# Optimization experiments

Measured on AMD Instinct MI355X. Metric: run time of the kernel, lower is better.

The kernel has to match this reference:

```python
import jax, jax.numpy as jnp
import numpy as np
from jax import lax

B, CIN, H, W = 2, 512, 64, 64
CD = CIN // 2            # down_dim = 256
CQ = CD // 8             # q/k channels = 32
EPS = 1e-5               # BatchNorm eps


def _conv3(x, w, b):
    # 3x3 conv, stride 1, padding 1 (init padding=1), NCHW/OIHW
    y = lax.conv_general_dilated(x, w, (1, 1), [(1, 1), (1, 1)],
                                 dimension_numbers=('NCHW', 'OIHW', 'NCHW'))
    return y + b[None, :, None, None]


def _bn(x, g, b, m, v):
    scale = g / jnp.sqrt(v + EPS)
    return x * scale[None, :, None, None] + (b - m * scale)[None, :, None, None]


def _prelu(x, a):
    return jnp.where(x > 0, x, a * x)


def _p1(x, w, b):
    # 1x1 conv as channel matmul
    return jnp.einsum('bchw,oc->bohw', x, w) + b[None, :, None, None]


def setup_inputs() -> dict:
    key = jax.random.key(0)
    it = iter(jax.random.split(key, 64))
    def nrm(shape, s=0.05):
        return jax.random.normal(next(it), shape, jnp.float32) * s
    inp = {
        'input_rgb': jax.random.normal(next(it), (B, CIN, H, W), jnp.float32),
        'input_dsm': jax.random.normal(next(it), (B, CIN, H, W), jnp.float32),
    }
    for m in ('rgb', 'dsm'):
        inp['conv_w_' + m] = nrm((CD, CIN, 3, 3))
        inp['conv_b_' + m] = nrm((CD,))
        inp['bn_g_' + m] = 1.0 + nrm((CD,))
        inp['bn_b_' + m] = nrm((CD,))
        inp['bn_m_' + m] = nrm((CD,))
        inp['bn_v_' + m] = jax.random.uniform(next(it), (CD,), jnp.float32, 0.5, 1.5)
        inp['prelu_' + m] = jnp.float32(0.25)
        inp['q_w_' + m] = nrm((CQ, CD)); inp['q_b_' + m] = nrm((CQ,))
        inp['k_w_' + m] = nrm((CQ, CD)); inp['k_b_' + m] = nrm((CQ,))
        inp['v_w_' + m] = nrm((CD, CD)); inp['v_b_' + m] = nrm((CD,))
        inp['up_w_' + m] = nrm((CIN, CD)); inp['up_b_' + m] = nrm((CIN,))
        inp['gamma_' + m] = jnp.float32(0.1)  # learned residual gate (zero-init in torch)
    return inp


def reference(input_rgb, input_dsm,
              conv_w_rgb, conv_b_rgb, bn_g_rgb, bn_b_rgb, bn_m_rgb, bn_v_rgb, prelu_rgb,
              q_w_rgb, q_b_rgb, k_w_rgb, k_b_rgb, v_w_rgb, v_b_rgb, up_w_rgb, up_b_rgb, gamma_rgb,
              conv_w_dsm, conv_b_dsm, bn_g_dsm, bn_b_dsm, bn_m_dsm, bn_v_dsm, prelu_dsm,
              q_w_dsm, q_b_dsm, k_w_dsm, k_b_dsm, v_w_dsm, v_b_dsm, up_w_dsm, up_b_dsm, gamma_dsm):
    conv_rgb = _prelu(_bn(_conv3(input_rgb, conv_w_rgb, conv_b_rgb),
                          bn_g_rgb, bn_b_rgb, bn_m_rgb, bn_v_rgb), prelu_rgb)
    conv_dsm = _prelu(_bn(_conv3(input_dsm, conv_w_dsm, conv_b_dsm),
                          bn_g_dsm, bn_b_dsm, bn_m_dsm, bn_v_dsm), prelu_dsm)
    b, c, h, w = conv_rgb.shape
    n = h * w
    q_rgb = _p1(conv_rgb, q_w_rgb, q_b_rgb).reshape(b, CQ, n)
    k_rgb = _p1(conv_rgb, k_w_rgb, k_b_rgb).reshape(b, CQ, n)
    v_rgb = _p1(conv_rgb, v_w_rgb, v_b_rgb).reshape(b, c, n)
    q_dsm = _p1(conv_dsm, q_w_dsm, q_b_dsm).reshape(b, CQ, n)
    k_dsm = _p1(conv_dsm, k_w_dsm, k_b_dsm).reshape(b, CQ, n)
    v_dsm = _p1(conv_dsm, v_w_dsm, v_b_dsm).reshape(b, c, n)
    # cross-modal unscaled attention: dsm queries attend over rgb keys
    attn_rgb = jax.nn.softmax(jnp.einsum('bqn,bqm->bnm', q_dsm, k_rgb), axis=-1)  # [b,n,n]
    o_rgb = jnp.einsum('bcj,bij->bci', v_rgb, attn_rgb).reshape(b, c, h, w)
    o_rgb = gamma_rgb * o_rgb + conv_rgb
    attn_dsm = jax.nn.softmax(jnp.einsum('bqn,bqm->bnm', q_rgb, k_dsm), axis=-1)
    o_dsm = jnp.einsum('bcj,bij->bci', v_dsm, attn_dsm).reshape(b, c, h, w)
    o_dsm = gamma_dsm * o_dsm + conv_dsm
    out_rgb = _p1(o_rgb, up_w_rgb, up_b_rgb) + input_rgb
    out_dsm = _p1(o_dsm, up_w_dsm, up_b_dsm) + input_dsm
    return (out_rgb, out_dsm)
```

## Files before the change

kernel.cpp:

```cpp
#include <hip/hip_runtime.h>
#include <hip/hip_bf16.h>
#include <stdint.h>


constexpr int CINCH = 512;
constexpr int NPIX  = 4096;

typedef __bf16 bf16x8 __attribute__((ext_vector_type(8)));
typedef __bf16 bf16x4 __attribute__((ext_vector_type(4)));
typedef float  f32x4  __attribute__((ext_vector_type(4)));

__device__ __forceinline__ __bf16 f2b(float f) {
    __hip_bfloat16 h = __float2bfloat16(f);
    return *reinterpret_cast<__bf16*>(&h);
}

__device__ __forceinline__ void load_lds16(const void* g, void* l) {
    __builtin_amdgcn_global_load_lds(
        (const __attribute__((address_space(1))) unsigned int*)(uintptr_t)g,
        (__attribute__((address_space(3))) unsigned int*)(uintptr_t)l,
        16, 0, 0);
}

__global__ __launch_bounds__(256)
void prep_w(const float* __restrict__ w_r, const float* __restrict__ w_d,
            const float* __restrict__ cb_r, const float* __restrict__ bg_r,
            const float* __restrict__ bb_r, const float* __restrict__ bm_r,
            const float* __restrict__ bv_r,
            const float* __restrict__ cb_d, const float* __restrict__ bg_d,
            const float* __restrict__ bb_d, const float* __restrict__ bm_d,
            const float* __restrict__ bv_d,
            __bf16* __restrict__ Wt, float* __restrict__ scA,
            float* __restrict__ shB, __bf16* __restrict__ zrow)
{
    const int t = threadIdx.x;
    const int blk = blockIdx.x;
    if (blk < 2304) {
        int gid = blk * 1024 + t * 4;
        int mod = gid >= 1179648;
        int o2  = gid - mod * 1179648;
        int tap = o2 >> 17;
        int r   = o2 & 131071;
        int oc  = r >> 9;
        int ic  = r & 511;
        const float* wsrc = mod ? w_d : w_r;
        long base = ((long)(oc * 512 + ic)) * 9 + tap;
        bf16x4 v;
        v.x = f2b(wsrc[base]);
        v.y = f2b(wsrc[base + 9]);
        v.z = f2b(wsrc[base + 18]);
        v.w = f2b(wsrc[base + 27]);
        *(bf16x4*)&Wt[gid] = v;
    } else if (blk == 2304) {
        unsigned short* z = (unsigned short*)zrow;
        z[t] = 0; z[t + 256] = 0;
    } else {
        int mod = blk - 2305;
        const float* cb = mod ? cb_d : cb_r;
        const float* bg = mod ? bg_d : bg_r;
        const float* bb = mod ? bb_d : bb_r;
        const float* bm = mod ? bm_d : bm_r;
        const float* bv = mod ? bv_d : bv_r;
        int oc = t;
        float sc = bg[oc] * rsqrtf(bv[oc] + 1e-5f);
        scA[mod * 256 + oc] = sc;
        shB[mod * 256 + oc] = (cb[oc] - bm[oc]) * sc + bb[oc];
    }
}

__global__ __launch_bounds__(256)
void prep_gw(const float* __restrict__ qw_r, const float* __restrict__ qw_d,
             const float* __restrict__ kw_r, const float* __restrict__ kw_d,
             const float* __restrict__ vw_r, const float* __restrict__ vw_d,
             const float* __restrict__ uw_r, const float* __restrict__ uw_d,
             __bf16* __restrict__ Wq, __bf16* __restrict__ Wk,
             __bf16* __restrict__ Wv, __bf16* __restrict__ Wu)
{
    int gid = blockIdx.x * 1024 + threadIdx.x * 4;
    __bf16* dst;
    float4 f = make_float4(0.f, 0.f, 0.f, 0.f);
    if (gid < 65536) {
        int mod = gid >> 15, e = gid & 32767;
        dst = Wq + gid;
        if (e < 8192) f = *(const float4*)((mod ? qw_d : qw_r) + e);
    } else if (gid < 131072) {
        int g = gid - 65536;
        int mod = g >> 15, e = g & 32767;
        dst = Wk + g;
        if (e < 8192) f = *(const float4*)((mod ? kw_d : kw_r) + e);
    } else if (gid < 262144) {
        int g = gid - 131072;
        int mod = g >> 16, e = g & 65535;
        dst = Wv + g;
        f = *(const float4*)((mod ? vw_d : vw_r) + e);
    } else {
        int g = gid - 262144;
        int mod = g >> 17, e = g & 131071;
        dst = Wu + g;
        f = *(const float4*)((mod ? uw_d : uw_r) + e);
    }
    bf16x4 o; o.x = f2b(f.x); o.y = f2b(f.y); o.z = f2b(f.z); o.w = f2b(f.w);
    *(bf16x4*)dst = o;
}

__global__ __launch_bounds__(256)
void xpose(const float* __restrict__ inr, const float* __restrict__ ind,
           __bf16* __restrict__ Xp)
{
    __shared__ float tile[32][33];
    const int t = threadIdx.x;
    const int p0 = blockIdx.x * 32;
    const int ic0 = blockIdx.y * 32;
    const int mb = blockIdx.z;
    const int mod = mb >> 1, b = mb & 1;
    const float* src = (mod ? ind : inr) + (long)b * CINCH * NPIX;

    int i = t >> 3, j4 = (t & 7) * 4;
    float4 v = *(const float4*)&src[(long)(ic0 + i) * NPIX + p0 + j4];
    tile[i][j4 + 0] = v.x; tile[i][j4 + 1] = v.y;
    tile[i][j4 + 2] = v.z; tile[i][j4 + 3] = v.w;
    __syncthreads();
    int j = t >> 3, i4 = (t & 7) * 4;
    bf16x4 o;
    o.x = f2b(tile[i4 + 0][j]);
    o.y = f2b(tile[i4 + 1][j]);
    o.z = f2b(tile[i4 + 2][j]);
    o.w = f2b(tile[i4 + 3][j]);
    *(bf16x4*)&Xp[((long)mb * NPIX + p0 + j) * 512 + ic0 + i4] = o;
}

__global__ __launch_bounds__(256)
void t256(const float* __restrict__ src, __bf16* __restrict__ dst)
{
    __shared__ float tile[32][33];
    const int t = threadIdx.x;
    const int p0 = blockIdx.x * 32;
    const int c0 = blockIdx.y * 32;
    const int mb = blockIdx.z;
    const float* s = src + (long)mb * 256 * NPIX;
    __bf16* d = dst + (long)mb * NPIX * 256;

    int i = t >> 3, j4 = (t & 7) * 4;
    float4 v = *(const float4*)&s[(long)(c0 + i) * NPIX + p0 + j4];
    tile[i][j4 + 0] = v.x; tile[i][j4 + 1] = v.y;
    tile[i][j4 + 2] = v.z; tile[i][j4 + 3] = v.w;
    __syncthreads();
    int j = t >> 3, i4 = (t & 7) * 4;
    bf16x4 o;
    o.x = f2b(tile[i4 + 0][j]); o.y = f2b(tile[i4 + 1][j]);
    o.z = f2b(tile[i4 + 2][j]); o.w = f2b(tile[i4 + 3][j]);
    *(bf16x4*)&d[((long)(p0 + j)) * 256 + c0 + i4] = o;
}

__global__ __launch_bounds__(512)
void conv_mfma(const __bf16* __restrict__ Wt, const __bf16* __restrict__ Xp,
               const __bf16* __restrict__ zrow, const float* __restrict__ scA,
               const float* __restrict__ shB, const float* __restrict__ prr,
               const float* __restrict__ prd, float* __restrict__ conv)
{
    __shared__ __bf16 As[3 * 64 * 64];
    __shared__ __bf16 Bs[2 * 385 * 64];

    const int t = threadIdx.x;
    const int y0 = blockIdx.x * 4;
    const int m0 = blockIdx.y * 64;
    const int mb = blockIdx.z;
    const int mod = mb >> 1;

    const __bf16* Am = Wt + (long)mod * (9 * 256 * 512);
    const __bf16* Xb = Xp + (long)mb * NPIX * 512;

    const int lane = t & 63, quad = lane >> 4, l15 = lane & 15, w = t >> 6;
    const int wy = w & 3, wo = w >> 2;

    if (t < 16)
        *(f32x4*)((char*)Bs + (t >> 3) * 49280 + 49152 + (t & 7) * 16) = (f32x4)0.f;
    asm volatile("s_waitcnt lgkmcnt(0)" ::: "memory");

    auto stage_a = [&](int buf, int tap, int cc) {
        int r  = w * 8 + (lane >> 3);
        int sl = (lane & 7) ^ (r & 7);
        const __bf16* src = Am + (long)tap * 131072 + (long)(m0 + r) * 512
                          + cc * 64 + sl * 8;
        load_lds16(src, (char*)As + buf * 8192 + w * 1024);
    };
    auto stage_b = [&](int buf, int cc) {
#pragma unroll
        for (int k = 0; k < 6; ++k) {
            int r  = w * 48 + k * 8 + (lane >> 3);
            int sl = (lane & 7) ^ (r & 7);
            int hr = r >> 6, xx = r & 63;
            int gy = y0 + hr - 1;
            const __bf16* src = ((unsigned)gy < 64u)
                ? Xb + (long)(gy * 64 + xx) * 512 + cc * 64 + sl * 8
                : zrow + sl * 8;
            load_lds16(src, (char*)Bs + buf * 49280 + (w * 48 + k * 8) * 128);
        }
    };

    f32x4 acc[2][4];
#pragma unroll
    for (int i = 0; i < 2; ++i)
#pragma unroll
        for (int j = 0; j < 4; ++j) acc[i][j] = (f32x4)0.f;

    stage_b(0, 0);
    stage_a(0, 0, 0);
    stage_a(1, 1, 0);

    const int soffA0 = ((quad ^ (l15 & 7)) << 4);
    const int soffA1 = (((4 | quad) ^ (l15 & 7)) << 4);

    for (int c = 0; c < 8; ++c) {
        for (int tp = 0; tp < 9; ++tp) {
            const int s = c * 9 + tp;
            if (s == 71)                  { asm volatile("s_waitcnt vmcnt(0)" ::: "memory"); }
            else if (tp >= 7 && c < 7)    { asm volatile("s_waitcnt vmcnt(7)" ::: "memory"); }
            else                          { asm volatile("s_waitcnt vmcnt(1)" ::: "memory"); }
            __builtin_amdgcn_sched_barrier(0);
            __builtin_amdgcn_s_barrier();
            __builtin_amdgcn_sched_barrier(0);

            if (s + 2 < 72) {
                int c2 = (tp + 2 >= 9) ? c + 1 : c;
                int t2 = (tp + 2 >= 9) ? tp - 7 : tp + 2;
                int b2 = (s + 2) % 3;
                stage_a(b2, t2, c2);
            }
            __builtin_amdgcn_sched_barrier(0);
            if (tp == 6 && c < 7) stage_b((c + 1) & 1, c + 1);
            __builtin_amdgcn_sched_barrier(0);

            const char* ab = (const char*)As + (s % 3) * 8192;
            const char* bb = (const char*)Bs + (c & 1) * 49280;
            const int dy = tp / 3 - 1, dx = tp % 3 - 1;
            const int hr = wy + 1 + dy;
            int rb[4];
#pragma unroll
            for (int fj = 0; fj < 4; ++fj) {
                int x = fj * 16 + l15 + dx;
                rb[fj] = ((unsigned)x < 64u) ? hr * 64 + x : 384;
            }
#pragma unroll
            for (int kk = 0; kk < 2; ++kk) {
                const int slq = kk * 4 + quad;
                bf16x8 af[2], bfr[4];
#pragma unroll
                for (int i = 0; i < 2; ++i)
                    af[i] = *(const bf16x8*)(ab + (wo * 32 + 16 * i + l15) * 128
                                             + (kk ? soffA1 : soffA0));
#pragma unroll
                for (int fj = 0; fj < 4; ++fj)
                    bfr[fj] = *(const bf16x8*)(bb + rb[fj] * 128
                                               + ((slq ^ (rb[fj] & 7)) << 4));
#pragma unroll
                for (int i = 0; i < 2; ++i)
#pragma unroll
                    for (int fj = 0; fj < 4; ++fj)
                        acc[i][fj] = __builtin_amdgcn_mfma_f32_16x16x32_bf16(
                            af[i], bfr[fj], acc[i][fj], 0, 0, 0);
            }
        }
    }

    const float alpha = (mod ? prd : prr)[0];
    float* outp = conv + (long)mb * 256 * NPIX;
    const int nbase = (y0 + wy) * 64;
#pragma unroll
    for (int i = 0; i < 2; ++i) {
#pragma unroll
        for (int r = 0; r < 4; ++r) {
            int oc = m0 + wo * 32 + 16 * i + quad * 4 + r;
            float sc = scA[mod * 256 + oc];
            float sh = shB[mod * 256 + oc];
            float* orow = outp + (long)oc * NPIX;
#pragma unroll
            for (int fj = 0; fj < 4; ++fj) {
                int n = nbase + 16 * fj + l15;
                float y = acc[i][fj][r] * sc + sh;
                y = (y > 0.f) ? y : alpha * y;
                orow[n] = y;
            }
        }
    }
}

__global__ __launch_bounds__(256)
void proj_mfma(const __bf16* __restrict__ Wb, int mstride,
               const __bf16* __restrict__ Bt,
               const float* __restrict__ bias_r, const float* __restrict__ bias_d,
               __bf16* __restrict__ dstT, __bf16* __restrict__ dstV,
               float* __restrict__ dstU,
               const float* __restrict__ resid_r, const float* __restrict__ resid_d,
               int mode, float oscale)
{
    __shared__ __bf16 As[128 * 32];
    __shared__ __bf16 Bs[128 * 32];

    const int t = threadIdx.x;
    const int n0 = blockIdx.x * 128;
    const int m0 = blockIdx.y * 128;
    const int mb = blockIdx.z;
    const int mod = mb >> 1, b = mb & 1;

    const __bf16* Am = Wb + (long)mod * mstride;
    const __bf16* Bm = Bt + (long)mb * (NPIX * 256);
    const float* bias = mod ? bias_d : bias_r;

    const int rowa = t >> 2, c16 = t & 3;
    char* ldsA0 = (char*)As + (t >> 6) * 1024;
    char* ldsA1 = ldsA0 + 4096;
    char* ldsB0 = (char*)Bs + (t >> 6) * 1024;
    char* ldsB1 = ldsB0 + 4096;
    const __bf16* srcA = Am + (long)(m0 + rowa) * 256 + c16 * 8;
    const __bf16* srcB = Bm + (long)(n0 + rowa) * 256 + c16 * 8;

    const int lane = t & 63, quad = lane >> 4, l15 = lane & 15, w = t >> 6;
    const int mw = (w >> 1) * 64, nw = (w & 1) * 64;
    const char* abase = (const char*)As + (mw + l15) * 64 + quad * 16;
    const char* bbase = (const char*)Bs + (nw + l15) * 64 + quad * 16;

    f32x4 acc[4][4];
#pragma unroll
    for (int i = 0; i < 4; ++i)
#pragma unroll
        for (int j = 0; j < 4; ++j) acc[i][j] = (f32x4)0.f;

    for (int kc = 0; kc < 256; kc += 32) {
        load_lds16(srcA + kc, ldsA0);
        load_lds16(srcA + kc + 16384, ldsA1);
        load_lds16(srcB + kc, ldsB0);
        load_lds16(srcB + kc + 16384, ldsB1);
        __syncthreads();

        bf16x8 af[4], bfr[4];
#pragma unroll
        for (int i = 0; i < 4; ++i) af[i]  = *(const bf16x8*)(abase + i * 1024);
#pragma unroll
        for (int j = 0; j < 4; ++j) bfr[j] = *(const bf16x8*)(bbase + j * 1024);
#pragma unroll
        for (int i = 0; i < 4; ++i)
#pragma unroll
            for (int j = 0; j < 4; ++j)
                acc[i][j] = __builtin_amdgcn_mfma_f32_16x16x32_bf16(
                    af[i], bfr[j], acc[i][j], 0, 0, 0);
        __syncthreads();
    }

    if (mode == 0) {
        if (mw == 0) {
            __bf16* dbase = dstT + (long)mb * (NPIX * 32);
#pragma unroll
            for (int fi = 0; fi < 2; ++fi)
#pragma unroll
                for (int r = 0; r < 4; ++r) {
                    int oc = 16 * fi + quad * 4 + r;
                    float bi = bias[oc];
#pragma unroll
                    for (int fj = 0; fj < 4; ++fj) {
                        int n = n0 + nw + 16 * fj + l15;
                        dbase[(long)n * 32 + oc] = f2b((acc[fi][fj][r] + bi) * oscale);
                    }
                }
        }
    } else if (mode == 1) {
        __bf16* dv = dstV + (long)mb * (256 * NPIX);
#pragma unroll
        for (int fi = 0; fi < 4; ++fi)
#pragma unroll
            for (int r = 0; r < 4; ++r) {
                int c = m0 + mw + 16 * fi + quad * 4 + r;
                float bi = bias[c];
                __bf16* row = dv + (long)c * NPIX;
#pragma unroll
                for (int fj = 0; fj < 4; ++fj) {
                    int n = n0 + nw + 16 * fj + l15;
                    row[n] = f2b(acc[fi][fj][r] + bi);
                }
            }
    } else {
        float* du = dstU + (long)mod * 4194304 + (long)b * 2097152;
        const float* rs = (mod ? resid_d : resid_r) + (long)b * 2097152;
#pragma unroll
        for (int fi = 0; fi < 4; ++fi)
#pragma unroll
            for (int r = 0; r < 4; ++r) {
                int oc = m0 + mw + 16 * fi + quad * 4 + r;
                float bi = bias[oc];
                const float* rrow = rs + (long)oc * NPIX;
                float* orow = du + (long)oc * NPIX;
#pragma unroll
                for (int fj = 0; fj < 4; ++fj) {
                    int n = n0 + nw + 16 * fj + l15;
                    orow[n] = acc[fi][fj][r] + bi + rrow[n];
                }
            }
    }
}

__global__ __launch_bounds__(256)
void attn_stats_mfma(const __bf16* __restrict__ Qt, const __bf16* __restrict__ Kt,
                     float* __restrict__ rmp)
{
    __shared__ __bf16 Qs[128 * 32];
    __shared__ __bf16 Ks[128 * 32];
    __shared__ float redm[2][128];

    const int t  = threadIdx.x;
    const int i0 = blockIdx.x * 128;
    const int mbo = blockIdx.y;
    const int o  = mbo >> 1, b = mbo & 1;
    const int seg = blockIdx.z;
    const int jbase = seg * 1024;
    const int mbK = o * 2 + b, mbQ = (1 - o) * 2 + b;

    const __bf16* Qg = Qt + (long)mbQ * 131072;
    const __bf16* Kg = Kt + (long)mbK * 131072;

    const int lane = t & 63, quad = lane >> 4, l15 = lane & 15, w = t >> 6;
    const int mS = (w >> 1) * 64;
    const int nS = (w & 1) * 64;

    const int drow = w * 16 + (lane >> 2);
    const int ssl  = ((lane & 3) ^ ((lane >> 3) & 3)) * 16;
    const int rsl  = (quad ^ ((l15 >> 1) & 3)) << 4;

    load_lds16((const char*)Qg + (long)(i0 + drow) * 64 + ssl, (char*)Qs + w * 1024);
    load_lds16((const char*)Qg + (long)(i0 + 64 + drow) * 64 + ssl,
               (char*)Qs + 4096 + w * 1024);
    __syncthreads();

    bf16x8 qa[4];
#pragma unroll
    for (int fi = 0; fi < 4; ++fi)
        qa[fi] = *(const bf16x8*)((const char*)Qs + (mS + 16 * fi + l15) * 64 + rsl);

    const f32x4 zero4 = (f32x4)0.f;
    float m_t[16];
#pragma unroll
    for (int e = 0; e < 16; ++e) m_t[e] = -3.0e38f;

    for (int j0 = jbase; j0 < jbase + 1024; j0 += 128) {
        __syncthreads();
        load_lds16((const char*)Kg + (long)(j0 + drow) * 64 + ssl, (char*)Ks + w * 1024);
        load_lds16((const char*)Kg + (long)(j0 + 64 + drow) * 64 + ssl,
                   (char*)Ks + 4096 + w * 1024);
        __syncthreads();

        bf16x8 kb[4];
#pragma unroll
        for (int fj = 0; fj < 4; ++fj)
            kb[fj] = *(const bf16x8*)((const char*)Ks + (nS + 16 * fj + l15) * 64 + rsl);
#pragma unroll
        for (int fi = 0; fi < 4; ++fi) {
            f32x4 sf[4];
#pragma unroll
            for (int fj = 0; fj < 4; ++fj)
                sf[fj] = __builtin_amdgcn_mfma_f32_16x16x32_bf16(qa[fi], kb[fj], zero4, 0, 0, 0);
#pragma unroll
            for (int r = 0; r < 4; ++r) {
                int e = fi * 4 + r;
                float a = fmaxf(fmaxf(sf[0][r], sf[1][r]), fmaxf(sf[2][r], sf[3][r]));
                m_t[e] = fmaxf(m_t[e], a);
            }
        }
    }

#pragma unroll
    for (int d = 1; d < 16; d <<= 1)
#pragma unroll
        for (int e = 0; e < 16; ++e)
            m_t[e] = fmaxf(m_t[e], __shfl_xor(m_t[e], d, 64));
    if (l15 == 0) {
#pragma unroll
        for (int fi = 0; fi < 4; ++fi)
#pragma unroll
            for (int r = 0; r < 4; ++r)
                redm[w & 1][mS + 16 * fi + quad * 4 + r] = m_t[fi * 4 + r];
    }
    __syncthreads();
    if (t < 128)
        rmp[seg * 16384 + mbo * 4096 + i0 + t] = fmaxf(redm[0][t], redm[1][t]);
}

__global__ __launch_bounds__(256)
void stats_merge(const float* __restrict__ rmp, float* __restrict__ rmb)
{
    int idx = blockIdx.x * 256 + threadIdx.x;
    float m = rmp[idx];
#pragma unroll
    for (int s = 1; s < 4; ++s) m = fmaxf(m, rmp[s * 16384 + idx]);
    rmb[idx] = m;
}

__global__ __launch_bounds__(256, 2)
void attn_pv_mfma(const __bf16* __restrict__ Qt, const __bf16* __restrict__ Kt,
                  const __bf16* __restrict__ Vb,
                  float* __restrict__ part0, float* __restrict__ part1,
                  const float* __restrict__ rmb, float* __restrict__ lbuf)
{
    __shared__ __bf16 Qs[64 * 32];
    __shared__ __bf16 Ks[64 * 32];
    __shared__ __bf16 Vs[2 * 256 * 32];
    __shared__ __bf16 Ps[64 * 64];

    const int t  = threadIdx.x;
    const int bx = blockIdx.x;
    const int grp = bx & 7;
    const int i0  = (bx >> 3) * 64;
    const int seg = grp & 1;
    const int mb  = grp >> 1;
    const int o  = mb >> 1, b = mb & 1;
    const int mbQ = (1 - o) * 2 + b;
    const int jbase = seg * 2048;

    const __bf16* Qg = Qt + (long)mbQ * 131072;
    const __bf16* Kg = Kt + (long)mb * 131072;
    const __bf16* Vg = Vb + (long)mb * 1048576;
    const float* rm = rmb + mb * 4096;

    const int lane = t & 63, quad = lane >> 4, l15 = lane & 15, w = t >> 6;
    const int iS = w * 16;
    const int cw = w * 64;

    const int drow = w * 16 + (lane >> 2);
    const int ssl  = ((lane & 3) ^ ((lane >> 3) & 3)) * 16;
    const int rsl  = (quad ^ ((l15 >> 1) & 3)) << 4;

    load_lds16((const char*)Qg + (long)(i0 + drow) * 64 + ssl, (char*)Qs + w * 1024);

    float mlv[4], lsum[4];
#pragma unroll
    for (int r = 0; r < 4; ++r) { mlv[r] = rm[i0 + iS + quad * 4 + r]; lsum[r] = 0.f; }

    f32x4 acc[4][4];
#pragma unroll
    for (int i = 0; i < 4; ++i)
#pragma unroll
        for (int j = 0; j < 4; ++j) acc[i][j] = (f32x4)0.f;
    const f32x4 zero4 = (f32x4)0.f;

    __syncthreads();
    const bf16x8 qa = *(const bf16x8*)((const char*)Qs + (iS + l15) * 64 + rsl);

    for (int j0 = jbase; j0 < jbase + 2048; j0 += 64) {
        __syncthreads();
        load_lds16((const char*)Kg + (long)(j0 + drow) * 64 + ssl,
                   (char*)Ks + w * 1024);
        __syncthreads();

#pragma unroll
        for (int ii = 0; ii < 8; ++ii) {
            int ks = ii >> 2;
            int c  = (ii & 3) * 64 + drow;
            load_lds16((const char*)Vg + (long)c * 8192 + (long)(j0 + ks * 32) * 2 + ssl,
                       (char*)Vs + ii * 4096 + w * 1024);
        }

        f32x4 sA[4];
#pragma unroll
        for (int fj = 0; fj < 4; ++fj) {
            bf16x8 kb = *(const bf16x8*)((const char*)Ks + (16 * fj + l15) * 64 + rsl);
            sA[fj] = __builtin_amdgcn_mfma_f32_16x16x32_bf16(qa, kb, zero4, 0, 0, 0);
        }
#pragma unroll
        for (int fj = 0; fj < 4; ++fj)
#pragma unroll
            for (int r = 0; r < 4; ++r) {
                int il = iS + quad * 4 + r;
                float p = exp2f(sA[fj][r] - mlv[r]);
                lsum[r] += p;
                int boff = (il * 128 + (16 * fj + l15) * 2) ^ ((il & 7) << 4);
                *(__bf16*)((char*)Ps + boff) = f2b(p);
            }
        __syncthreads();

#pragma unroll
        for (int ks = 0; ks < 2; ++ks) {
            bf16x8 va[4], pb[4];
#pragma unroll
            for (int fi = 0; fi < 4; ++fi)
                va[fi] = *(const bf16x8*)((const char*)Vs + ks * 16384 +
                                          (cw + 16 * fi + l15) * 64 + rsl);
#pragma unroll
            for (int fj = 0; fj < 4; ++fj) {
                int ip = 16 * fj + l15;
                int boff = (ip * 128 + ks * 64 + quad * 16) ^ ((ip & 7) << 4);
                pb[fj] = *(const bf16x8*)((const char*)Ps + boff);
            }
#pragma unroll
            for (int fi = 0; fi < 4; ++fi)
#pragma unroll
                for (int fj = 0; fj < 4; ++fj)
                    acc[fi][fj] = __builtin_amdgcn_mfma_f32_16x16x32_bf16(
                        va[fi], pb[fj], acc[fi][fj], 0, 0, 0);
        }
    }

    float* pg = (seg ? part1 : part0) + (long)mb * 1048576;
#pragma unroll
    for (int fi = 0; fi < 4; ++fi) {
#pragma unroll
        for (int r = 0; r < 4; ++r) {
            int c = cw + 16 * fi + quad * 4 + r;
            float* zr = pg + (long)c * 4096;
#pragma unroll
            for (int fj = 0; fj < 4; ++fj)
                zr[i0 + 16 * fj + l15] = acc[fi][fj][r];
        }
    }

#pragma unroll
    for (int d = 1; d < 16; d <<= 1)
#pragma unroll
        for (int r = 0; r < 4; ++r)
            lsum[r] += __shfl_xor(lsum[r], d, 64);
    if (l15 == 0) {
        float* lb = lbuf + seg * 16384 + mb * 4096;
#pragma unroll
        for (int r = 0; r < 4; ++r)
            lb[i0 + iS + quad * 4 + r] = lsum[r];
    }
}

__global__ __launch_bounds__(256)
void zred_t(const float* __restrict__ p0, const float* __restrict__ p1,
            const float* __restrict__ convb, __bf16* __restrict__ Zt,
            const float* __restrict__ g_r, const float* __restrict__ g_d,
            const float* __restrict__ lbuf)
{
    __shared__ float tile[32][33];
    const int t = threadIdx.x;
    const int pix0 = blockIdx.x * 32;
    const int c0 = blockIdx.y * 32;
    const int mb = blockIdx.z;
    const int o = mb >> 1;
    const float gamma = (o ? g_d : g_r)[0];
    const long base = (long)mb * 1048576;

    int i = t >> 3, j4 = (t & 7) * 4;
    const float* l0p = lbuf + mb * 4096;
    const float* l1p = lbuf + 16384 + mb * 4096;
    float4 la = *(const float4*)&l0p[pix0 + j4];
    float4 lc = *(const float4*)&l1p[pix0 + j4];
    float g0 = gamma / (la.x + lc.x);
    float g1 = gamma / (la.y + lc.y);
    float g2 = gamma / (la.z + lc.z);
    float g3 = gamma / (la.w + lc.w);

    long row = base + (long)(c0 + i) * 4096 + pix0 + j4;
    float4 a = *(const float4*)&p0[row];
    float4 b = *(const float4*)&p1[row];
    float4 cv = *(const float4*)&convb[row];
    tile[i][j4 + 0] = g0 * (a.x + b.x) + cv.x;
    tile[i][j4 + 1] = g1 * (a.y + b.y) + cv.y;
    tile[i][j4 + 2] = g2 * (a.z + b.z) + cv.z;
    tile[i][j4 + 3] = g3 * (a.w + b.w) + cv.w;
    __syncthreads();
    int j = t >> 3, i4 = (t & 7) * 4;
    bf16x4 oq;
    oq.x = f2b(tile[i4 + 0][j]); oq.y = f2b(tile[i4 + 1][j]);
    oq.z = f2b(tile[i4 + 2][j]); oq.w = f2b(tile[i4 + 3][j]);
    *(bf16x4*)&Zt[(long)mb * NPIX * 256 + (long)(pix0 + j) * 256 + c0 + i4] = oq;
}

extern "C" void kernel_launch(void* const* d_in, const int* in_sizes, int n_in,
                              void* d_out, int out_size, void* d_ws, size_t ws_size,
                              hipStream_t stream)
{
    const float* in_rgb = (const float*)d_in[0];
    const float* in_dsm = (const float*)d_in[1];
    auto P = [&](int i) { return (const float*)d_in[i]; };

    float* ws    = (float*)d_ws;
    float* conv  = ws;
    float* part0 = ws + 4194304;
    float* rmb   = ws + 8388608;
    float* lbuf  = ws + 8421376;
    float* rmp   = part0;
    float* scA   = ws + 8486912;
    float* shB   = ws + 8487424;
    __bf16* zrow = (__bf16*)(ws + 8487936);
    __bf16* Wt   = (__bf16*)(ws + 8488192);
    __bf16* Xp   = (__bf16*)(ws + 9667840);
    float*  part1 = ws + 9667840;
    __bf16* Qt   = (__bf16*)(ws + 13862144);
    __bf16* Kt   = (__bf16*)(ws + 14124288);
    __bf16* Vbb  = (__bf16*)(ws + 14386432);
    __bf16* Ct   = (__bf16*)(ws + 16483584);
    __bf16* Zt   = (__bf16*)(ws + 18580736);
    __bf16* Wq   = (__bf16*)(ws + 20677888);
    __bf16* Wk   = (__bf16*)(ws + 20710656);
    __bf16* Wv   = (__bf16*)(ws + 20743424);
    __bf16* Wu   = (__bf16*)(ws + 20808960);

    prep_w<<<2307, 256, 0, stream>>>(
        P(2), P(18), P(3), P(4), P(5), P(6), P(7),
        P(19), P(20), P(21), P(22), P(23),
        Wt, scA, shB, zrow);
    prep_gw<<<512, 256, 0, stream>>>(
        P(9), P(25), P(11), P(27), P(13), P(29), P(15), P(31),
        Wq, Wk, Wv, Wu);
    xpose<<<dim3(128, 16, 4), 256, 0, stream>>>(in_rgb, in_dsm, Xp);

    conv_mfma<<<dim3(16, 4, 4), 512, 0, stream>>>(
        Wt, Xp, zrow, scA, shB, P(8), P(24), conv);
    t256<<<dim3(128, 8, 4), 256, 0, stream>>>(conv, Ct);

    proj_mfma<<<dim3(32, 1, 4), 256, 0, stream>>>(
        Wq, 32768, Ct, P(10), P(26), Qt, nullptr, nullptr, nullptr, nullptr,
        0, 1.4426950408889634f);
    proj_mfma<<<dim3(32, 1, 4), 256, 0, stream>>>(
        Wk, 32768, Ct, P(12), P(28), Kt, nullptr, nullptr, nullptr, nullptr,
        0, 1.0f);
    proj_mfma<<<dim3(32, 2, 4), 256, 0, stream>>>(
        Wv, 65536, Ct, P(14), P(30), nullptr, Vbb, nullptr, nullptr, nullptr,
        1, 1.0f);

    attn_stats_mfma<<<dim3(32, 4, 4), 256, 0, stream>>>(Qt, Kt, rmp);
    stats_merge<<<64, 256, 0, stream>>>(rmp, rmb);

    attn_pv_mfma<<<512, 256, 0, stream>>>(
        Qt, Kt, Vbb, part0, part1, rmb, lbuf);

    zred_t<<<dim3(128, 8, 4), 256, 0, stream>>>(
        part0, part1, conv, Zt, P(17), P(33), lbuf);

    proj_mfma<<<dim3(32, 4, 4), 256, 0, stream>>>(
        Wu, 131072, Zt, P(16), P(32), nullptr, nullptr, (float*)d_out,
        in_rgb, in_dsm, 2, 1.0f);
}
```

Before: 333.0 us.

## Write conv output directly as transposed bf16 and drop transpose kernel

The conv kernel now writes its post-BN/PReLU result directly into the pixel-major bf16 buffer Ct, which removes the separate t256 transpose kernel and the fp32 conv buffer. The residual in zred_t now reads from bf16 Ct, so the conv residual carries bf16 precision. Separately, the attention PV kernel builds its row sums from the bf16 P fragments loaded for the MFMA instead of accumulating in the exp loop, which shortens the shuffle reduction. The direct epilogue stores are strided 2-byte scatters, so they may be poorly coalesced.

Result: slower. 404.9 us (+21.6%).

```diff
diff --git a/kernel.cpp b/kernel.cpp
--- a/kernel.cpp
+++ b/kernel.cpp
@@ -129,34 +129,11 @@
     *(bf16x4*)&Xp[((long)mb * NPIX + p0 + j) * 512 + ic0 + i4] = o;
 }
 
-__global__ __launch_bounds__(256)
-void t256(const float* __restrict__ src, __bf16* __restrict__ dst)
-{
-    __shared__ float tile[32][33];
-    const int t = threadIdx.x;
-    const int p0 = blockIdx.x * 32;
-    const int c0 = blockIdx.y * 32;
-    const int mb = blockIdx.z;
-    const float* s = src + (long)mb * 256 * NPIX;
-    __bf16* d = dst + (long)mb * NPIX * 256;
-
-    int i = t >> 3, j4 = (t & 7) * 4;
-    float4 v = *(const float4*)&s[(long)(c0 + i) * NPIX + p0 + j4];
-    tile[i][j4 + 0] = v.x; tile[i][j4 + 1] = v.y;
-    tile[i][j4 + 2] = v.z; tile[i][j4 + 3] = v.w;
-    __syncthreads();
-    int j = t >> 3, i4 = (t & 7) * 4;
-    bf16x4 o;
-    o.x = f2b(tile[i4 + 0][j]); o.y = f2b(tile[i4 + 1][j]);
-    o.z = f2b(tile[i4 + 2][j]); o.w = f2b(tile[i4 + 3][j]);
-    *(bf16x4*)&d[((long)(p0 + j)) * 256 + c0 + i4] = o;
-}
-
 __global__ __launch_bounds__(512)
 void conv_mfma(const __bf16* __restrict__ Wt, const __bf16* __restrict__ Xp,
                const __bf16* __restrict__ zrow, const float* __restrict__ scA,
                const float* __restrict__ shB, const float* __restrict__ prr,
-               const float* __restrict__ prd, float* __restrict__ conv)
+               const float* __restrict__ prd, __bf16* __restrict__ Ct)
 {
     __shared__ __bf16 As[3 * 64 * 64];
     __shared__ __bf16 Bs[2 * 385 * 64];
@@ -264,7 +241,7 @@
     }
 
     const float alpha = (mod ? prd : prr)[0];
-    float* outp = conv + (long)mb * 256 * NPIX;
+    __bf16* ctp = Ct + (long)mb * (NPIX * 256);
     const int nbase = (y0 + wy) * 64;
 #pragma unroll
     for (int i = 0; i < 2; ++i) {
@@ -273,13 +250,12 @@
             int oc = m0 + wo * 32 + 16 * i + quad * 4 + r;
             float sc = scA[mod * 256 + oc];
             float sh = shB[mod * 256 + oc];
-            float* orow = outp + (long)oc * NPIX;
 #pragma unroll
             for (int fj = 0; fj < 4; ++fj) {
                 int n = nbase + 16 * fj + l15;
                 float y = acc[i][fj][r] * sc + sh;
                 y = (y > 0.f) ? y : alpha * y;
-                orow[n] = y;
+                ctp[(long)n * 256 + oc] = f2b(y);
             }
         }
     }
@@ -529,9 +505,10 @@
 
     load_lds16((const char*)Qg + (long)(i0 + drow) * 64 + ssl, (char*)Qs + w * 1024);
 
-    float mlv[4], lsum[4];
-#pragma unroll
-    for (int r = 0; r < 4; ++r) { mlv[r] = rm[i0 + iS + quad * 4 + r]; lsum[r] = 0.f; }
+    float mlv[4];
+#pragma unroll
+    for (int r = 0; r < 4; ++r) mlv[r] = rm[i0 + iS + quad * 4 + r];
+    float lsum = 0.f;
 
     f32x4 acc[4][4];
 #pragma unroll
@@ -568,10 +545,8 @@
 #pragma unroll
             for (int r = 0; r < 4; ++r) {
                 int il = iS + quad * 4 + r;
-                float p = exp2f(sA[fj][r] - mlv[r]);
-                lsum[r] += p;
                 int boff = (il * 128 + (16 * fj + l15) * 2) ^ ((il & 7) << 4);
-                *(__bf16*)((char*)Ps + boff) = f2b(p);
+                *(__bf16*)((char*)Ps + boff) = f2b(exp2f(sA[fj][r] - mlv[r]));
             }
         __syncthreads();
 
@@ -588,6 +563,11 @@
                 int boff = (ip * 128 + ks * 64 + quad * 16) ^ ((ip & 7) << 4);
                 pb[fj] = *(const bf16x8*)((const char*)Ps + boff);
             }
+            {
+                bf16x8 pw = pb[w];
+#pragma unroll
+                for (int e = 0; e < 8; ++e) lsum += (float)pw[e];
+            }
 #pragma unroll
             for (int fi = 0; fi < 4; ++fi)
 #pragma unroll
@@ -610,22 +590,15 @@
         }
     }
 
-#pragma unroll
-    for (int d = 1; d < 16; d <<= 1)
-#pragma unroll
-        for (int r = 0; r < 4; ++r)
-            lsum[r] += __shfl_xor(lsum[r], d, 64);
-    if (l15 == 0) {
-        float* lb = lbuf + seg * 16384 + mb * 4096;
-#pragma unroll
-        for (int r = 0; r < 4; ++r)
-            lb[i0 + iS + quad * 4 + r] = lsum[r];
-    }
+    lsum += __shfl_xor(lsum, 16, 64);
+    lsum += __shfl_xor(lsum, 32, 64);
+    if (quad == 0)
+        lbuf[seg * 16384 + mb * 4096 + i0 + 16 * w + l15] = lsum;
 }
 
 __global__ __launch_bounds__(256)
 void zred_t(const float* __restrict__ p0, const float* __restrict__ p1,
-            const float* __restrict__ convb, __bf16* __restrict__ Zt,
+            const __bf16* __restrict__ Ct, __bf16* __restrict__ Zt,
             const float* __restrict__ g_r, const float* __restrict__ g_d,
             const float* __restrict__ lbuf)
 {
@@ -651,16 +624,19 @@
     long row = base + (long)(c0 + i) * 4096 + pix0 + j4;
     float4 a = *(const float4*)&p0[row];
     float4 b = *(const float4*)&p1[row];
-    float4 cv = *(const float4*)&convb[row];
-    tile[i][j4 + 0] = g0 * (a.x + b.x) + cv.x;
-    tile[i][j4 + 1] = g1 * (a.y + b.y) + cv.y;
-    tile[i][j4 + 2] = g2 * (a.z + b.z) + cv.z;
-    tile[i][j4 + 3] = g3 * (a.w + b.w) + cv.w;
+    tile[i][j4 + 0] = g0 * (a.x + b.x);
+    tile[i][j4 + 1] = g1 * (a.y + b.y);
+    tile[i][j4 + 2] = g2 * (a.z + b.z);
+    tile[i][j4 + 3] = g3 * (a.w + b.w);
     __syncthreads();
     int j = t >> 3, i4 = (t & 7) * 4;
+    bf16x4 cv = *(const bf16x4*)&Ct[(long)mb * NPIX * 256 +
+                                    (long)(pix0 + j) * 256 + c0 + i4];
     bf16x4 oq;
-    oq.x = f2b(tile[i4 + 0][j]); oq.y = f2b(tile[i4 + 1][j]);
-    oq.z = f2b(tile[i4 + 2][j]); oq.w = f2b(tile[i4 + 3][j]);
+    oq.x = f2b(tile[i4 + 0][j] + (float)cv.x);
+    oq.y = f2b(tile[i4 + 1][j] + (float)cv.y);
+    oq.z = f2b(tile[i4 + 2][j] + (float)cv.z);
+    oq.w = f2b(tile[i4 + 3][j] + (float)cv.w);
     *(bf16x4*)&Zt[(long)mb * NPIX * 256 + (long)(pix0 + j) * 256 + c0 + i4] = oq;
 }
 
@@ -673,7 +649,6 @@
     auto P = [&](int i) { return (const float*)d_in[i]; };
 
     float* ws    = (float*)d_ws;
-    float* conv  = ws;
     float* part0 = ws + 4194304;
     float* rmb   = ws + 8388608;
     float* lbuf  = ws + 8421376;
@@ -704,8 +679,7 @@
     xpose<<<dim3(128, 16, 4), 256, 0, stream>>>(in_rgb, in_dsm, Xp);
 
     conv_mfma<<<dim3(16, 4, 4), 512, 0, stream>>>(
-        Wt, Xp, zrow, scA, shB, P(8), P(24), conv);
-    t256<<<dim3(128, 8, 4), 256, 0, stream>>>(conv, Ct);
+        Wt, Xp, zrow, scA, shB, P(8), P(24), Ct);
 
     proj_mfma<<<dim3(32, 1, 4), 256, 0, stream>>>(
         Wq, 32768, Ct, P(10), P(26), Qt, nullptr, nullptr, nullptr, nullptr,
@@ -724,7 +698,7 @@
         Qt, Kt, Vbb, part0, part1, rmb, lbuf);
 
     zred_t<<<dim3(128, 8, 4), 256, 0, stream>>>(
-        part0, part1, conv, Zt, P(17), P(33), lbuf);
+        part0, part1, Ct, Zt, P(17), P(33), lbuf);
 
     proj_mfma<<<dim3(32, 4, 4), 256, 0, stream>>>(
         Wu, 131072, Zt, P(16), P(32), nullptr, nullptr, (float*)d_out,
```
